# Kernel optimization log

Hardware: AMD Instinct MI355X
Metric: run time of the kernel (lower is better)

Reference implementation:

```python
import jax, jax.numpy as jnp
import numpy as np
import math

E = 1024      # embed_dim
H = 16        # num_heads
D = 32        # head_dim = E // H // 2
DEPTH = 12
LAMBDA_INIT = 0.8 - 0.6 * math.exp(-0.3 * DEPTH)
B, T = 4, 1024
EPS = 1e-5


def setup_inputs() -> dict:
    key = jax.random.key(0)
    ks = jax.random.split(key, 10)
    s = 0.02  # realistic init scale for weight matrices
    return {
        "x": jax.random.normal(ks[0], (B, T, E), jnp.float32),
        "Wq": jax.random.normal(ks[1], (E, E), jnp.float32) * s,
        "Wk": jax.random.normal(ks[2], (E, E), jnp.float32) * s,
        "Wv": jax.random.normal(ks[3], (E, E), jnp.float32) * s,
        "Wo": jax.random.normal(ks[4], (E, E), jnp.float32) * s,
        "lambda_q1": jax.random.normal(ks[5], (D,), jnp.float32) * 0.1,
        "lambda_k1": jax.random.normal(ks[6], (D,), jnp.float32) * 0.1,
        "lambda_q2": jax.random.normal(ks[7], (D,), jnp.float32) * 0.1,
        "lambda_k2": jax.random.normal(ks[8], (D,), jnp.float32) * 0.1,
        "g": jnp.ones((2 * D,), jnp.float32),  # subln affine weight
    }


def reference(x, Wq, Wk, Wv, Wo, lambda_q1, lambda_k1, lambda_q2, lambda_k2, g):
    b, t, _ = x.shape
    scaling = D ** -0.5
    # projections (torch Linear: x @ W.T), split into 2H half-width q/k heads
    q = (x @ Wq.T).reshape(b, t, 2 * H, D).transpose(0, 2, 1, 3) * scaling  # [b,2H,t,D]
    k = (x @ Wk.T).reshape(b, t, 2 * H, D).transpose(0, 2, 1, 3)            # [b,2H,t,D]
    v = (x @ Wv.T).reshape(b, t, H, 2 * D).transpose(0, 2, 1, 3)            # [b,H,t,2D]
    # dual score maps, fp32 softmax
    aw = jnp.einsum('bhqd,bhkd->bhqk', q, k)               # [b,2H,t,t]
    aw = jnp.nan_to_num(aw)
    aw = jax.nn.softmax(aw.astype(jnp.float32), axis=-1).astype(q.dtype)
    # scalar lambda
    lam1 = jnp.exp(jnp.sum(lambda_q1 * lambda_k1))
    lam2 = jnp.exp(jnp.sum(lambda_q2 * lambda_k2))
    lam = lam1 - lam2 + LAMBDA_INIT
    # differential subtract of the paired softmax maps
    aw = aw.reshape(b, H, 2, t, t)
    aw = aw[:, :, 0] - lam * aw[:, :, 1]                   # [b,H,t,t]
    attn = jnp.einsum('bhqk,bhkd->bhqd', aw, v)            # [b,H,t,2D]
    # per-head RMSNorm over 2D channel dim (affine)
    attn = attn * jax.lax.rsqrt(jnp.mean(attn * attn, axis=-1, keepdims=True) + EPS) * g
    attn = attn * (1.0 - LAMBDA_INIT)
    attn = attn.transpose(0, 2, 1, 3).reshape(b, t, H * 2 * D)  # [b,t,E]
    return attn @ Wo.T
```

## Files before the change

### kernel.cpp

```cpp
#include <hip/hip_runtime.h>
#include <math.h>

#define E_   1024
#define H_   16
#define B_   4
#define T_   1024
#define LAMBDA_INIT 0.783605766532f
#define SCALE_Q 0.17677669529663687f
#define SK 68

typedef short s16x8 __attribute__((ext_vector_type(8)));
typedef float f32x4 __attribute__((ext_vector_type(4)));

__device__ inline ushort f2bf(float x) {
    unsigned u = __builtin_bit_cast(unsigned, x);
    u += 0x7fffu + ((u >> 16) & 1u);
    return (ushort)(u >> 16);
}

__device__ inline uint f2bf2(float lo, float hi) {
#if __has_builtin(__builtin_amdgcn_cvt_pk_bf16_f32)
    typedef __bf16 bf16x2_t __attribute__((ext_vector_type(2)));
    bf16x2_t r = __builtin_amdgcn_cvt_pk_bf16_f32(lo, hi);
    return __builtin_bit_cast(uint, r);
#else
    uint ul = __builtin_bit_cast(uint, lo);
    uint uh = __builtin_bit_cast(uint, hi);
    ul += 0x7fffu + ((ul >> 16) & 1u);
    uh += 0x7fffu + ((uh >> 16) & 1u);
    return __builtin_amdgcn_perm(uh, ul, 0x07060302u);
#endif
}

__device__ inline void gl_lds16(const ushort* g, ushort* l) {
    __builtin_amdgcn_global_load_lds((const __attribute__((address_space(1))) void*)g,
                                     (__attribute__((address_space(3))) void*)l,
                                     16, 0, 0);
}

__global__ __launch_bounds__(256) void prep(
    const float* __restrict__ x,  const float* __restrict__ Wq,
    const float* __restrict__ Wk, const float* __restrict__ Wv,
    const float* __restrict__ Wo,
    const float* __restrict__ lq1, const float* __restrict__ lk1,
    const float* __restrict__ lq2, const float* __restrict__ lk2,
    ushort* __restrict__ xb, ushort* __restrict__ Wqb, ushort* __restrict__ Wkb,
    ushort* __restrict__ Wvb, ushort* __restrict__ Wob, float* __restrict__ lamp)
{
    const int blk = blockIdx.x;
    const int tid = threadIdx.x;
    if (blk >= 4096) {
        if (tid < 64) {
            float p1 = 0.f, p2 = 0.f;
            if (tid < 32) { p1 = lq1[tid] * lk1[tid]; p2 = lq2[tid] * lk2[tid]; }
            #pragma unroll
            for (int off = 32; off; off >>= 1) {
                p1 += __shfl_xor(p1, off);
                p2 += __shfl_xor(p2, off);
            }
            if (tid == 0) lamp[0] = expf(p1) - expf(p2) + LAMBDA_INIT;
        }
        return;
    }
    const float* in;
    ushort* out;
    int base;
    if (blk < 2048) { in = x; out = xb; base = blk; }
    else {
        int t = blk - 2048, w = t >> 9;
        base = t & 511;
        in  = w == 0 ? Wq  : (w == 1 ? Wk  : (w == 2 ? Wv  : Wo));
        out = w == 0 ? Wqb : (w == 1 ? Wkb : (w == 2 ? Wvb : Wob));
    }
    int i = (base * 256 + tid) * 8;
    float4 a = *(const float4*)&in[i];
    float4 b = *(const float4*)&in[i + 4];
    union { ushort u[8]; uint4 v; } o;
    o.u[0] = f2bf(a.x); o.u[1] = f2bf(a.y); o.u[2] = f2bf(a.z); o.u[3] = f2bf(a.w);
    o.u[4] = f2bf(b.x); o.u[5] = f2bf(b.y); o.u[6] = f2bf(b.z); o.u[7] = f2bf(b.w);
    *(uint4*)&out[i] = o.v;
}

__global__ __launch_bounds__(256) void gemm_qkv(
    const ushort* __restrict__ Xb, const ushort* __restrict__ Wqb,
    const ushort* __restrict__ Wkb, const ushort* __restrict__ Wvb,
    ushort* __restrict__ QKV)
{
    __shared__ ushort As[128 * 32];
    __shared__ ushort Ws[128 * 32];
    const int tid = threadIdx.x;
    const int wave = tid >> 6, lane = tid & 63;
    const int l15 = lane & 15, quad = lane >> 4;
    const int bm = blockIdx.y * 128;
    const int bng = blockIdx.x * 128;
    const int region = bng >> 10;
    const ushort* W = region == 0 ? Wqb : (region == 1 ? Wkb : Wvb);
    const float scale = region == 0 ? SCALE_Q : 1.0f;
    const int wn = bng & 1023;
    const int lrow = lane >> 2;
    const int lcol = (lane & 3) * 8;

    f32x4 acc[4][4] = {};
    const int wr = wave >> 1, wc = wave & 1;

    for (int k0 = 0; k0 < 1024; k0 += 32) {
        #pragma unroll
        for (int p = 0; p < 2; ++p) {
            int i = wave + 4 * p;
            gl_lds16(&Xb[(size_t)(bm + i * 16 + lrow) * 1024 + k0 + lcol], &As[i * 512]);
            gl_lds16(&W [(size_t)(wn + i * 16 + lrow) * 1024 + k0 + lcol], &Ws[i * 512]);
        }
        __syncthreads();
        s16x8 a[4], b[4];
        #pragma unroll
        for (int i = 0; i < 4; ++i)
            a[i] = *(const s16x8*)&As[(wr * 64 + i * 16 + l15) * 32 + quad * 8];
        #pragma unroll
        for (int j = 0; j < 4; ++j)
            b[j] = *(const s16x8*)&Ws[(wc * 64 + j * 16 + l15) * 32 + quad * 8];
        #pragma unroll
        for (int i = 0; i < 4; ++i)
            #pragma unroll
            for (int j = 0; j < 4; ++j)
                acc[i][j] = __builtin_amdgcn_mfma_f32_16x16x32_bf16(a[i], b[j], acc[i][j], 0, 0, 0);
        __syncthreads();
    }

    #pragma unroll
    for (int i = 0; i < 4; ++i)
        #pragma unroll
        for (int j = 0; j < 4; ++j)
            #pragma unroll
            for (int r = 0; r < 4; ++r) {
                int row = bm + wr * 64 + i * 16 + quad * 4 + r;
                int col = bng + wc * 64 + j * 16 + l15;
                QKV[(size_t)row * 3072 + col] = f2bf(acc[i][j][r] * scale);
            }
}

__global__ __launch_bounds__(256) void gemm_out(
    const ushort* __restrict__ Ab, const ushort* __restrict__ Wob,
    float* __restrict__ C)
{
    __shared__ ushort As[64 * 32];
    __shared__ ushort Ws[128 * 32];
    const int tid = threadIdx.x;
    const int wave = tid >> 6, lane = tid & 63;
    const int l15 = lane & 15, quad = lane >> 4;
    const int bm = blockIdx.y * 64;
    const int bn = blockIdx.x * 128;
    const int lrow = lane >> 2;
    const int lcol = (lane & 3) * 8;

    f32x4 acc[2][4] = {};
    const int wr = wave >> 1, wc = wave & 1;

    for (int k0 = 0; k0 < 1024; k0 += 32) {
        gl_lds16(&Ab[(size_t)(bm + wave * 16 + lrow) * 1024 + k0 + lcol], &As[wave * 512]);
        #pragma unroll
        for (int p = 0; p < 2; ++p) {
            int i = wave + 4 * p;
            gl_lds16(&Wob[(size_t)(bn + i * 16 + lrow) * 1024 + k0 + lcol], &Ws[i * 512]);
        }
        __syncthreads();
        s16x8 a[2], b[4];
        #pragma unroll
        for (int i = 0; i < 2; ++i)
            a[i] = *(const s16x8*)&As[(wr * 32 + i * 16 + l15) * 32 + quad * 8];
        #pragma unroll
        for (int j = 0; j < 4; ++j)
            b[j] = *(const s16x8*)&Ws[(wc * 64 + j * 16 + l15) * 32 + quad * 8];
        #pragma unroll
        for (int i = 0; i < 2; ++i)
            #pragma unroll
            for (int j = 0; j < 4; ++j)
                acc[i][j] = __builtin_amdgcn_mfma_f32_16x16x32_bf16(a[i], b[j], acc[i][j], 0, 0, 0);
        __syncthreads();
    }

    #pragma unroll
    for (int i = 0; i < 2; ++i)
        #pragma unroll
        for (int j = 0; j < 4; ++j)
            #pragma unroll
            for (int r = 0; r < 4; ++r) {
                int row = bm + wr * 32 + i * 16 + quad * 4 + r;
                int col = bn + wc * 64 + j * 16 + l15;
                C[(size_t)row * 1024 + col] = acc[i][j][r];
            }
}

__global__ __launch_bounds__(256) void transpose_v(
    const ushort* __restrict__ QKV, ushort* __restrict__ Vt)
{
    __shared__ ushort Ls[64][72];
    const int tid = threadIdx.x;
    const int m0 = blockIdx.x * 64;
    const int b  = m0 >> 10;
    const int t0 = m0 & 1023;
    const int e0 = blockIdx.y * 64;
    #pragma unroll
    for (int p = 0; p < 2; ++p) {
        int idx = tid + 256 * p;
        int r = idx >> 3, seg = (idx & 7) * 8;
        *(uint4*)&Ls[r][seg] =
            *(const uint4*)&QKV[(size_t)(m0 + r) * 3072 + 2048 + e0 + seg];
    }
    __syncthreads();
    #pragma unroll
    for (int p = 0; p < 2; ++p) {
        int idx = tid + 256 * p;
        int er = idx >> 3, ts = (idx & 7) * 8;
        union { ushort u[8]; uint4 v; } o;
        #pragma unroll
        for (int i = 0; i < 8; ++i) o.u[i] = Ls[ts + i][er];
        *(uint4*)&Vt[((size_t)b * E_ + e0 + er) * T_ + t0 + ts] = o.v;
    }
}

__global__ __launch_bounds__(256, 4) void diff_attn(
    const ushort* __restrict__ QKV, const ushort* __restrict__ Vt,
    const float* __restrict__ g, const float* __restrict__ lamp,
    ushort* __restrict__ O)
{
    __shared__ __align__(16) ushort Ks[64 * SK];
    __shared__ __align__(16) ushort Vts[64 * SK];
    __shared__ __align__(16) ushort PtQ[4 * 2 * 16 * SK];

    const int tid  = threadIdx.x;
    const int lane = tid & 63;
    const int wave = tid >> 6;
    const int l15  = lane & 15;
    const int quad = lane >> 4;

    const int blk = blockIdx.x;
    const int qt = blk & 15;
    const int h  = (blk >> 4) & 15;
    const int b  = blk >> 8;
    const int q0 = qt * 64;
    const int hoff = h * 64;
    const size_t rowbase = (size_t)b * T_;
    const size_t vtbase = ((size_t)b * E_ + hoff) * T_;

    const ushort* Qg = QKV;
    const ushort* Kg = QKV + 1024;

    {
        int r = tid >> 2, seg = (tid & 3) * 16;
        *(uint4*)&PtQ[r * SK + seg] =
            *(const uint4*)&Qg[(rowbase + q0 + r) * 3072 + hoff + seg];
        *(uint4*)&PtQ[r * SK + seg + 8] =
            *(const uint4*)&Qg[(rowbase + q0 + r) * 3072 + hoff + seg + 8];
    }
    const float lam = lamp[0];
    float4 gv[4];
    #pragma unroll
    for (int jt = 0; jt < 4; ++jt) gv[jt] = *(const float4*)&g[jt * 16 + quad * 4];
    __syncthreads();

    s16x8 aq[2];
    #pragma unroll
    for (int c = 0; c < 2; ++c)
        aq[c] = *(const s16x8*)&PtQ[(wave * 16 + l15) * SK + c * 32 + quad * 8];
    __syncthreads();

    ushort* Pt0 = &PtQ[(wave * 2 + 0) * 16 * SK];
    ushort* Pt1 = &PtQ[(wave * 2 + 1) * 16 * SK];

    const f32x4 zf = {0.f, 0.f, 0.f, 0.f};
    f32x4 o0[4] = {zf, zf, zf, zf};
    f32x4 o1[4] = {zf, zf, zf, zf};
    float lsum[2] = {0.f, 0.f};

    const int r0 = tid >> 2, s0 = (tid & 3) * 16;
    uint4 kr0, kr1, vr0, vr1;
    {
        size_t ko = (rowbase + 0 + r0) * 3072 + hoff + s0;
        kr0 = *(const uint4*)&Kg[ko];
        kr1 = *(const uint4*)&Kg[ko + 8];
        size_t vo = vtbase + (size_t)r0 * T_ + 0 + s0;
        vr0 = *(const uint4*)&Vt[vo];
        vr1 = *(const uint4*)&Vt[vo + 8];
    }

    for (int kt = 0; kt < T_ / 64; ++kt) {
        __syncthreads();
        *(uint4*)&Ks[r0 * SK + s0]      = kr0;
        *(uint4*)&Ks[r0 * SK + s0 + 8]  = kr1;
        *(uint4*)&Vts[r0 * SK + s0]     = vr0;
        *(uint4*)&Vts[r0 * SK + s0 + 8] = vr1;
        __syncthreads();

        {
            int ktn = (kt + 1) & 15;
            size_t ko = (rowbase + ktn * 64 + r0) * 3072 + hoff + s0;
            kr0 = *(const uint4*)&Kg[ko];
            kr1 = *(const uint4*)&Kg[ko + 8];
            size_t vo = vtbase + (size_t)r0 * T_ + ktn * 64 + s0;
            vr0 = *(const uint4*)&Vt[vo];
            vr1 = *(const uint4*)&Vt[vo + 8];
        }

        f32x4 S0[4], S1[4];
        #pragma unroll
        for (int jk = 0; jk < 4; ++jk) {
            s16x8 ka0 = *(const s16x8*)&Ks[(jk * 16 + l15) * SK + quad * 8];
            s16x8 ka1 = *(const s16x8*)&Ks[(jk * 16 + l15) * SK + 32 + quad * 8];
            S0[jk] = __builtin_amdgcn_mfma_f32_16x16x32_bf16(ka0, aq[0], zf, 0, 0, 0);
            S1[jk] = __builtin_amdgcn_mfma_f32_16x16x32_bf16(ka1, aq[1], zf, 0, 0, 0);
        }
        float part0 = 0.f, part1 = 0.f;
        #pragma unroll
        for (int jk = 0; jk < 4; ++jk) {
            float a0 = __expf(S0[jk][0]), a1 = __expf(S0[jk][1]);
            float a2 = __expf(S0[jk][2]), a3 = __expf(S0[jk][3]);
            float b0 = __expf(S1[jk][0]), b1 = __expf(S1[jk][1]);
            float b2 = __expf(S1[jk][2]), b3 = __expf(S1[jk][3]);
            part0 += (a0 + a1) + (a2 + a3);
            part1 += (b0 + b1) + (b2 + b3);
            uint2 pk0, pk1;
            pk0.x = f2bf2(a0, a1); pk0.y = f2bf2(a2, a3);
            pk1.x = f2bf2(b0, b1); pk1.y = f2bf2(b2, b3);
            *(uint2*)&Pt0[l15 * SK + jk * 16 + quad * 4] = pk0;
            *(uint2*)&Pt1[l15 * SK + jk * 16 + quad * 4] = pk1;
        }
        lsum[0] += part0;
        lsum[1] += part1;
        #pragma unroll
        for (int h2 = 0; h2 < 2; ++h2) {
            s16x8 pf0 = *(const s16x8*)&Pt0[l15 * SK + h2 * 32 + quad * 8];
            s16x8 pf1 = *(const s16x8*)&Pt1[l15 * SK + h2 * 32 + quad * 8];
            #pragma unroll
            for (int jt = 0; jt < 4; ++jt) {
                s16x8 va = *(const s16x8*)&Vts[(jt * 16 + l15) * SK + h2 * 32 + quad * 8];
                o0[jt] = __builtin_amdgcn_mfma_f32_16x16x32_bf16(va, pf0, o0[jt], 0, 0, 0);
                o1[jt] = __builtin_amdgcn_mfma_f32_16x16x32_bf16(va, pf1, o1[jt], 0, 0, 0);
            }
        }
    }

    #pragma unroll
    for (int c = 0; c < 2; ++c) {
        float s = lsum[c];
        s += __shfl_xor(s, 16);
        s += __shfl_xor(s, 32);
        lsum[c] = s;
    }

    const float fin = 1.f - LAMBDA_INIT;
    float i0 = 1.f / lsum[0];
    float i1 = lam / lsum[1];
    float val[4][4];
    float ssq = 0.f;
    #pragma unroll
    for (int jt = 0; jt < 4; ++jt)
        #pragma unroll
        for (int r = 0; r < 4; ++r) {
            float v = o0[jt][r] * i0 - o1[jt][r] * i1;
            val[jt][r] = v;
            ssq += v * v;
        }
    ssq += __shfl_xor(ssq, 16);
    ssq += __shfl_xor(ssq, 32);
    float sc = rsqrtf(ssq * (1.f / 64.f) + 1e-5f) * fin;
    size_t rowoff = (rowbase + q0 + wave * 16 + l15) * 1024 + hoff;
    #pragma unroll
    for (int jt = 0; jt < 4; ++jt) {
        uint p01 = f2bf2(val[jt][0] * sc * gv[jt].x, val[jt][1] * sc * gv[jt].y);
        uint p23 = f2bf2(val[jt][2] * sc * gv[jt].z, val[jt][3] * sc * gv[jt].w);
        *(uint*)&O[rowoff + jt * 16 + quad * 4 + 0] = p01;
        *(uint*)&O[rowoff + jt * 16 + quad * 4 + 2] = p23;
    }
}

extern "C" void kernel_launch(void* const* d_in, const int* in_sizes, int n_in,
                              void* d_out, int out_size, void* d_ws, size_t ws_size,
                              hipStream_t stream)
{
    const float* x   = (const float*)d_in[0];
    const float* Wq  = (const float*)d_in[1];
    const float* Wk  = (const float*)d_in[2];
    const float* Wv  = (const float*)d_in[3];
    const float* Wo  = (const float*)d_in[4];
    const float* lq1 = (const float*)d_in[5];
    const float* lk1 = (const float*)d_in[6];
    const float* lq2 = (const float*)d_in[7];
    const float* lk2 = (const float*)d_in[8];
    const float* g   = (const float*)d_in[9];
    float* out = (float*)d_out;

    const int M = B_ * T_;
    const size_t ME = (size_t)M * E_;
    const size_t EE = (size_t)E_ * E_;
    ushort* xb  = (ushort*)d_ws;
    ushort* Wqb = xb  + ME;
    ushort* Wkb = Wqb + EE;
    ushort* Wvb = Wkb + EE;
    ushort* Wob = Wvb + EE;
    ushort* QKV = Wob + EE;
    ushort* Vtb = QKV + (size_t)M * 3072;
    ushort* Ab  = Vtb + ME;
    float*  lamp = (float*)(Ab + ME);

    prep<<<4097, 256, 0, stream>>>(x, Wq, Wk, Wv, Wo, lq1, lk1, lq2, lk2,
                                   xb, Wqb, Wkb, Wvb, Wob, lamp);
    gemm_qkv<<<dim3(24, 32), 256, 0, stream>>>(xb, Wqb, Wkb, Wvb, QKV);
    transpose_v<<<dim3(M / 64, E_ / 64), 256, 0, stream>>>(QKV, Vtb);
    diff_attn<<<B_ * H_ * (T_ / 64), 256, 0, stream>>>(QKV, Vtb, g, lamp, Ab);
    gemm_out<<<dim3(8, 64), 256, 0, stream>>>(Ab, Wob, out);
}
```

Before: 214.2 us.

## Fuse V transpose into QKV GEMM epilogue and load K/V directly from global

The QKV GEMM now writes V straight into the transposed Vt layout, which removes the separate transpose kernel and one launch. The attention kernel no longer stages K and V tiles in shared memory with block barriers. Each wave reads its K and Vt fragments directly from global or L2, and the grid order is changed so that blocks sharing a (batch, head) run close together for L2 reuse. Occupancy is raised to 5 blocks per SM. The risks are uncoalesced 16-byte global loads of K with a 3072-element stride, and redundant K/V reads across the four waves in place of shared-memory reuse.

```diff
diff --git a/kernel.cpp b/kernel.cpp
--- a/kernel.cpp
+++ b/kernel.cpp
@@ -84,7 +84,7 @@
 __global__ __launch_bounds__(256) void gemm_qkv(
     const ushort* __restrict__ Xb, const ushort* __restrict__ Wqb,
     const ushort* __restrict__ Wkb, const ushort* __restrict__ Wvb,
-    ushort* __restrict__ QKV)
+    ushort* __restrict__ QKV, ushort* __restrict__ Vt)
 {
     __shared__ ushort As[128 * 32];
     __shared__ ushort Ws[128 * 32];
@@ -126,16 +126,31 @@
         __syncthreads();
     }
 
-    #pragma unroll
-    for (int i = 0; i < 4; ++i)
-        #pragma unroll
-        for (int j = 0; j < 4; ++j)
-            #pragma unroll
-            for (int r = 0; r < 4; ++r) {
-                int row = bm + wr * 64 + i * 16 + quad * 4 + r;
-                int col = bng + wc * 64 + j * 16 + l15;
-                QKV[(size_t)row * 3072 + col] = f2bf(acc[i][j][r] * scale);
+    if (region < 2) {
+        #pragma unroll
+        for (int i = 0; i < 4; ++i)
+            #pragma unroll
+            for (int j = 0; j < 4; ++j)
+                #pragma unroll
+                for (int r = 0; r < 4; ++r) {
+                    int row = bm + wr * 64 + i * 16 + quad * 4 + r;
+                    int col = bng + wc * 64 + j * 16 + l15;
+                    QKV[(size_t)row * 3072 + col] = f2bf(acc[i][j][r] * scale);
+                }
+    } else {
+        const int bb = bm >> 10;
+        const int t0 = (bm & 1023) + wr * 64 + quad * 4;
+        #pragma unroll
+        for (int i = 0; i < 4; ++i)
+            #pragma unroll
+            for (int j = 0; j < 4; ++j) {
+                int e = wn + wc * 64 + j * 16 + l15;
+                ushort4 o;
+                o.x = f2bf(acc[i][j][0]); o.y = f2bf(acc[i][j][1]);
+                o.z = f2bf(acc[i][j][2]); o.w = f2bf(acc[i][j][3]);
+                *(ushort4*)&Vt[((size_t)bb * E_ + e) * T_ + t0 + i * 16] = o;
             }
+    }
 }
 
 __global__ __launch_bounds__(256) void gemm_out(
@@ -190,42 +205,12 @@
             }
 }
 
-__global__ __launch_bounds__(256) void transpose_v(
-    const ushort* __restrict__ QKV, ushort* __restrict__ Vt)
-{
-    __shared__ ushort Ls[64][72];
-    const int tid = threadIdx.x;
-    const int m0 = blockIdx.x * 64;
-    const int b  = m0 >> 10;
-    const int t0 = m0 & 1023;
-    const int e0 = blockIdx.y * 64;
-    #pragma unroll
-    for (int p = 0; p < 2; ++p) {
-        int idx = tid + 256 * p;
-        int r = idx >> 3, seg = (idx & 7) * 8;
-        *(uint4*)&Ls[r][seg] =
-            *(const uint4*)&QKV[(size_t)(m0 + r) * 3072 + 2048 + e0 + seg];
-    }
-    __syncthreads();
-    #pragma unroll
-    for (int p = 0; p < 2; ++p) {
-        int idx = tid + 256 * p;
-        int er = idx >> 3, ts = (idx & 7) * 8;
-        union { ushort u[8]; uint4 v; } o;
-        #pragma unroll
-        for (int i = 0; i < 8; ++i) o.u[i] = Ls[ts + i][er];
-        *(uint4*)&Vt[((size_t)b * E_ + e0 + er) * T_ + t0 + ts] = o.v;
-    }
-}
-
-__global__ __launch_bounds__(256, 4) void diff_attn(
+__global__ __launch_bounds__(256, 5) void diff_attn(
     const ushort* __restrict__ QKV, const ushort* __restrict__ Vt,
     const float* __restrict__ g, const float* __restrict__ lamp,
     ushort* __restrict__ O)
 {
-    __shared__ __align__(16) ushort Ks[64 * SK];
-    __shared__ __align__(16) ushort Vts[64 * SK];
-    __shared__ __align__(16) ushort PtQ[4 * 2 * 16 * SK];
+    __shared__ __align__(16) ushort Pt[4][2][16 * SK];
 
     const int tid  = threadIdx.x;
     const int lane = tid & 63;
@@ -234,122 +219,91 @@
     const int quad = lane >> 4;
 
     const int blk = blockIdx.x;
-    const int qt = blk & 15;
-    const int h  = (blk >> 4) & 15;
-    const int b  = blk >> 8;
+    const int bh = blk & 63;
+    const int qt = blk >> 6;
+    const int b  = bh >> 4;
+    const int h  = bh & 15;
     const int q0 = qt * 64;
     const int hoff = h * 64;
     const size_t rowbase = (size_t)b * T_;
-    const size_t vtbase = ((size_t)b * E_ + hoff) * T_;
 
     const ushort* Qg = QKV;
     const ushort* Kg = QKV + 1024;
-
-    {
-        int r = tid >> 2, seg = (tid & 3) * 16;
-        *(uint4*)&PtQ[r * SK + seg] =
-            *(const uint4*)&Qg[(rowbase + q0 + r) * 3072 + hoff + seg];
-        *(uint4*)&PtQ[r * SK + seg + 8] =
-            *(const uint4*)&Qg[(rowbase + q0 + r) * 3072 + hoff + seg + 8];
-    }
+    const ushort* Kbase = Kg + rowbase * 3072 + hoff;
+    const ushort* Vbase = Vt + ((size_t)b * E_ + hoff) * T_;
+
+    const size_t qrow = (rowbase + q0 + wave * 16 + l15) * 3072 + hoff;
+    s16x8 aq0 = *(const s16x8*)&Qg[qrow + quad * 8];
+    s16x8 aq1 = *(const s16x8*)&Qg[qrow + 32 + quad * 8];
+
     const float lam = lamp[0];
     float4 gv[4];
     #pragma unroll
     for (int jt = 0; jt < 4; ++jt) gv[jt] = *(const float4*)&g[jt * 16 + quad * 4];
-    __syncthreads();
-
-    s16x8 aq[2];
-    #pragma unroll
-    for (int c = 0; c < 2; ++c)
-        aq[c] = *(const s16x8*)&PtQ[(wave * 16 + l15) * SK + c * 32 + quad * 8];
-    __syncthreads();
-
-    ushort* Pt0 = &PtQ[(wave * 2 + 0) * 16 * SK];
-    ushort* Pt1 = &PtQ[(wave * 2 + 1) * 16 * SK];
+
+    ushort* Pt0 = &Pt[wave][0][0];
+    ushort* Pt1 = &Pt[wave][1][0];
 
     const f32x4 zf = {0.f, 0.f, 0.f, 0.f};
     f32x4 o0[4] = {zf, zf, zf, zf};
     f32x4 o1[4] = {zf, zf, zf, zf};
-    float lsum[2] = {0.f, 0.f};
-
-    const int r0 = tid >> 2, s0 = (tid & 3) * 16;
-    uint4 kr0, kr1, vr0, vr1;
-    {
-        size_t ko = (rowbase + 0 + r0) * 3072 + hoff + s0;
-        kr0 = *(const uint4*)&Kg[ko];
-        kr1 = *(const uint4*)&Kg[ko + 8];
-        size_t vo = vtbase + (size_t)r0 * T_ + 0 + s0;
-        vr0 = *(const uint4*)&Vt[vo];
-        vr1 = *(const uint4*)&Vt[vo + 8];
-    }
+    float lsum0 = 0.f, lsum1 = 0.f;
 
     for (int kt = 0; kt < T_ / 64; ++kt) {
-        __syncthreads();
-        *(uint4*)&Ks[r0 * SK + s0]      = kr0;
-        *(uint4*)&Ks[r0 * SK + s0 + 8]  = kr1;
-        *(uint4*)&Vts[r0 * SK + s0]     = vr0;
-        *(uint4*)&Vts[r0 * SK + s0 + 8] = vr1;
-        __syncthreads();
-
-        {
-            int ktn = (kt + 1) & 15;
-            size_t ko = (rowbase + ktn * 64 + r0) * 3072 + hoff + s0;
-            kr0 = *(const uint4*)&Kg[ko];
-            kr1 = *(const uint4*)&Kg[ko + 8];
-            size_t vo = vtbase + (size_t)r0 * T_ + ktn * 64 + s0;
-            vr0 = *(const uint4*)&Vt[vo];
-            vr1 = *(const uint4*)&Vt[vo + 8];
-        }
-
-        f32x4 S0[4], S1[4];
+        const ushort* Kt = Kbase + (size_t)kt * 64 * 3072;
+
+        f32x4 S0[4];
         #pragma unroll
         for (int jk = 0; jk < 4; ++jk) {
-            s16x8 ka0 = *(const s16x8*)&Ks[(jk * 16 + l15) * SK + quad * 8];
-            s16x8 ka1 = *(const s16x8*)&Ks[(jk * 16 + l15) * SK + 32 + quad * 8];
-            S0[jk] = __builtin_amdgcn_mfma_f32_16x16x32_bf16(ka0, aq[0], zf, 0, 0, 0);
-            S1[jk] = __builtin_amdgcn_mfma_f32_16x16x32_bf16(ka1, aq[1], zf, 0, 0, 0);
-        }
-        float part0 = 0.f, part1 = 0.f;
+            s16x8 ka = *(const s16x8*)&Kt[(size_t)(jk * 16 + l15) * 3072 + quad * 8];
+            S0[jk] = __builtin_amdgcn_mfma_f32_16x16x32_bf16(ka, aq0, zf, 0, 0, 0);
+        }
         #pragma unroll
         for (int jk = 0; jk < 4; ++jk) {
-            float a0 = __expf(S0[jk][0]), a1 = __expf(S0[jk][1]);
-            float a2 = __expf(S0[jk][2]), a3 = __expf(S0[jk][3]);
-            float b0 = __expf(S1[jk][0]), b1 = __expf(S1[jk][1]);
-            float b2 = __expf(S1[jk][2]), b3 = __expf(S1[jk][3]);
-            part0 += (a0 + a1) + (a2 + a3);
-            part1 += (b0 + b1) + (b2 + b3);
-            uint2 pk0, pk1;
-            pk0.x = f2bf2(a0, a1); pk0.y = f2bf2(a2, a3);
-            pk1.x = f2bf2(b0, b1); pk1.y = f2bf2(b2, b3);
-            *(uint2*)&Pt0[l15 * SK + jk * 16 + quad * 4] = pk0;
-            *(uint2*)&Pt1[l15 * SK + jk * 16 + quad * 4] = pk1;
-        }
-        lsum[0] += part0;
-        lsum[1] += part1;
+            float e0 = __expf(S0[jk][0]), e1 = __expf(S0[jk][1]);
+            float e2 = __expf(S0[jk][2]), e3 = __expf(S0[jk][3]);
+            lsum0 += (e0 + e1) + (e2 + e3);
+            uint2 pk;
+            pk.x = f2bf2(e0, e1); pk.y = f2bf2(e2, e3);
+            *(uint2*)&Pt0[l15 * SK + jk * 16 + quad * 4] = pk;
+        }
+
+        f32x4 S1[4];
+        #pragma unroll
+        for (int jk = 0; jk < 4; ++jk) {
+            s16x8 ka = *(const s16x8*)&Kt[(size_t)(jk * 16 + l15) * 3072 + 32 + quad * 8];
+            S1[jk] = __builtin_amdgcn_mfma_f32_16x16x32_bf16(ka, aq1, zf, 0, 0, 0);
+        }
+        #pragma unroll
+        for (int jk = 0; jk < 4; ++jk) {
+            float e0 = __expf(S1[jk][0]), e1 = __expf(S1[jk][1]);
+            float e2 = __expf(S1[jk][2]), e3 = __expf(S1[jk][3]);
+            lsum1 += (e0 + e1) + (e2 + e3);
+            uint2 pk;
+            pk.x = f2bf2(e0, e1); pk.y = f2bf2(e2, e3);
+            *(uint2*)&Pt1[l15 * SK + jk * 16 + quad * 4] = pk;
+        }
+
         #pragma unroll
         for (int h2 = 0; h2 < 2; ++h2) {
             s16x8 pf0 = *(const s16x8*)&Pt0[l15 * SK + h2 * 32 + quad * 8];
             s16x8 pf1 = *(const s16x8*)&Pt1[l15 * SK + h2 * 32 + quad * 8];
             #pragma unroll
             for (int jt = 0; jt < 4; ++jt) {
-                s16x8 va = *(const s16x8*)&Vts[(jt * 16 + l15) * SK + h2 * 32 + quad * 8];
+                s16x8 va = *(const s16x8*)&Vbase[(size_t)(jt * 16 + l15) * T_
+                                                 + kt * 64 + h2 * 32 + quad * 8];
                 o0[jt] = __builtin_amdgcn_mfma_f32_16x16x32_bf16(va, pf0, o0[jt], 0, 0, 0);
                 o1[jt] = __builtin_amdgcn_mfma_f32_16x16x32_bf16(va, pf1, o1[jt], 0, 0, 0);
             }
         }
     }
 
-    #pragma unroll
-    for (int c = 0; c < 2; ++c) {
-        float s = lsum[c];
-        s += __shfl_xor(s, 16);
-        s += __shfl_xor(s, 32);
-        lsum[c] = s;
-    }
+    lsum0 += __shfl_xor(lsum0, 16); lsum0 += __shfl_xor(lsum0, 32);
+    lsum1 += __shfl_xor(lsum1, 16); lsum1 += __shfl_xor(lsum1, 32);
 
     const float fin = 1.f - LAMBDA_INIT;
-    float i0 = 1.f / lsum[0];
-    float i1 = lam / lsum[1];
+    float i0 = 1.f / lsum0;
+    float i1 = lam / lsum1;
     float val[4][4];
     float ssq = 0.f;
     #pragma unroll
@@ -404,8 +358,7 @@
 
     prep<<<4097, 256, 0, stream>>>(x, Wq, Wk, Wv, Wo, lq1, lk1, lq2, lk2,
                                    xb, Wqb, Wkb, Wvb, Wob, lamp);
-    gemm_qkv<<<dim3(24, 32), 256, 0, stream>>>(xb, Wqb, Wkb, Wvb, QKV);
-    transpose_v<<<dim3(M / 64, E_ / 64), 256, 0, stream>>>(QKV, Vtb);
+    gemm_qkv<<<dim3(24, 32), 256, 0, stream>>>(xb, Wqb, Wkb, Wvb, QKV, Vtb);
     diff_attn<<<B_ * H_ * (T_ / 64), 256, 0, stream>>>(QKV, Vtb, g, lamp, Ab);
     gemm_out<<<dim3(8, 64), 256, 0, stream>>>(Ab, Wob, out);
 }
```

After: 298.2 us. +39.2%, slower.
